# Performance work log

Measured on AMD Instinct MI355X. Metric: run time of the kernel, lower is better.

Reference implementation:

```python
import jax, jax.numpy as jnp
import numpy as np

T = 2.0          # hardcoded in __init__ (self.T = 2)
EPSILON = 0.1    # sinkhorn_loss default
N_ITERS = 10     # sinkhorn_loss default passed to sinkhorn_normalized
COST_CLIP = 10.0
TINY = 1e-8

B, S, V = 16, 512, 4096


def setup_inputs() -> dict:
    key = jax.random.key(0)
    k1, k2 = jax.random.split(key)
    y_s = jax.random.normal(k1, (B, S, V), dtype=jnp.float32)
    y_t = jax.random.normal(k2, (B, S, V), dtype=jnp.float32)
    return {"y_s": y_s, "y_t": y_t}


def _cdist_l1(x, y):
    # x, y: [S, V] -> [S, S]; row-streamed via lax.map to avoid a [S,S,V] intermediate
    return jax.lax.map(lambda xi: jnp.sum(jnp.abs(xi[None, :] - y), axis=-1), x)


def _sinkhorn_loss(x, y):
    # x, y: [S, V] softmax probabilities for one sample
    Wxy = _cdist_l1(x, y)                                  # [S, S]
    K = jnp.exp(-jnp.minimum(Wxy, COST_CLIP) / EPSILON)
    P = jnp.nan_to_num(K, nan=TINY, posinf=1e6, neginf=-1e6) + TINY
    for _ in range(N_ITERS):
        P = P / jnp.maximum(jnp.sum(P, axis=1, keepdims=True), TINY)
        P = jnp.nan_to_num(P, nan=TINY)
        P = P / jnp.maximum(jnp.sum(P, axis=0, keepdims=True), TINY)
        P = jnp.nan_to_num(P, nan=TINY)
    return jnp.sum(P * Wxy)


def reference(y_s, y_t):
    p_s = jax.nn.softmax(y_s / T, axis=-1)
    p_t = jax.nn.softmax(y_t / T, axis=-1)
    p_s = jnp.nan_to_num(p_s, nan=TINY)
    p_t = jnp.nan_to_num(p_t, nan=TINY)
    per_sample = jax.vmap(_sinkhorn_loss)(p_s, p_t)        # [B]
    # forward accumulates 0.001 * loss_i and divides by the number of valid samples
    return jnp.mean(0.001 * per_sample)
```

## Files before the change

kernel.cpp:

```cpp
#include <hip/hip_runtime.h>

#define B_ 16
#define S_ 512
#define V_ 4096

typedef unsigned int uint;
typedef unsigned short ushort;
typedef unsigned char u8;


__device__ __forceinline__ uint sad8(uint a, uint b, uint c) {
#if __has_builtin(__builtin_amdgcn_sad_u8)
    return __builtin_amdgcn_sad_u8(a, b, c);
#else
    uint s = c;
#pragma unroll
    for (int i = 0; i < 4; ++i) {
        uint x = (a >> (8 * i)) & 0xFFu, y = (b >> (8 * i)) & 0xFFu;
        s += x > y ? x - y : y - x;
    }
    return s;
#endif
}

__device__ __forceinline__ float bflo(uint p) { return __uint_as_float(p << 16); }
__device__ __forceinline__ float bfhi(uint p) { return __uint_as_float(p & 0xFFFF0000u); }

__device__ __forceinline__ ushort f2bf(float f) {
    uint u = __float_as_uint(f);
    u = (u + 0x7FFFu + ((u >> 16) & 1u)) >> 16;
    return (ushort)u;
}

__device__ __forceinline__ float waveMax(float v) {
#pragma unroll
    for (int o = 32; o; o >>= 1) v = fmaxf(v, __shfl_xor(v, o, 64));
    return v;
}
__device__ __forceinline__ float waveSum(float v) {
#pragma unroll
    for (int o = 32; o; o >>= 1) v += __shfl_xor(v, o, 64);
    return v;
}

#define GLOAD_LDS16(g, l)                                                      \
    __builtin_amdgcn_global_load_lds(                                          \
        (const __attribute__((address_space(1))) uint*)(g),                    \
        (__attribute__((address_space(3))) uint*)(l), 16, 0, 0)

#define QSCALE 65536.0f
#define QINV   1.52587890625e-5f

__global__ __launch_bounds__(256) void softmax_kernel(
        const float* __restrict__ ys, const float* __restrict__ yt,
        u8* __restrict__ qs, u8* __restrict__ qt) {
    const int row = blockIdx.x;
    const float* in = blockIdx.y ? yt : ys;
    u8* out = blockIdx.y ? qt : qs;
    const float* px = in + (size_t)row * V_;
    u8* po = out + (size_t)row * V_;
    const int tid = threadIdx.x;

    float4 v4[4];
    float m = -3.4e38f;
#pragma unroll
    for (int i = 0; i < 4; ++i) {
        v4[i] = ((const float4*)px)[tid + 256 * i];
        m = fmaxf(m, fmaxf(fmaxf(v4[i].x, v4[i].y), fmaxf(v4[i].z, v4[i].w)));
    }
    __shared__ float redm[4], reds[4];
    float wm = waveMax(m);
    if ((tid & 63) == 0) redm[tid >> 6] = wm;
    __syncthreads();
    const float rm = fmaxf(fmaxf(redm[0], redm[1]), fmaxf(redm[2], redm[3]));

    float e[16];
    float s = 0.f;
#pragma unroll
    for (int i = 0; i < 4; ++i) {
        const float* f = (const float*)&v4[i];
#pragma unroll
        for (int k = 0; k < 4; ++k) {
            float ev = __expf((f[k] - rm) * 0.5f);
            e[i * 4 + k] = ev;
            s += ev;
        }
    }
    float wsm = waveSum(s);
    if ((tid & 63) == 0) reds[tid >> 6] = wsm;
    __syncthreads();
    const float inv = 1.0f / (reds[0] + reds[1] + reds[2] + reds[3]);

#pragma unroll
    for (int i = 0; i < 4; ++i) {
        uint pk = 0;
#pragma unroll
        for (int k = 0; k < 4; ++k) {
            float p = e[i * 4 + k] * inv;
            uint q = (uint)fminf(p * QSCALE + 0.5f, 255.f);
            pk |= q << (8 * k);
        }
        ((uint*)po)[tid + 256 * i] = pk;
    }
}

#define TI 64
#define TJ 64
#define KCB 64

__global__ __launch_bounds__(256) void pairwise_kernel(
        const u8* __restrict__ qs, const u8* __restrict__ qt,
        ushort* __restrict__ Wb, ushort* __restrict__ Kb) {
    const int b = blockIdx.z;
    const int tR = blockIdx.y * TI;
    const int tC = blockIdx.x * TJ;
    const u8* xrow = qs + (size_t)b * S_ * V_ + (size_t)tR * V_;
    const u8* yrow = qt + (size_t)b * S_ * V_ + (size_t)tC * V_;
    const int tid = threadIdx.x;
    const int lane = tid & 63, wv = tid >> 6;
    const int tx = tid & 15, ty = tid >> 4;

    __shared__ u8 xs[2][TI * KCB];
    __shared__ u8 ysm[2][TJ * KCB];

    const int rs = lane >> 2;
    const int coff = (((lane & 3) ^ ((lane >> 3) & 3)) << 4);
    const size_t gsrc = (size_t)(wv * 16 + rs) * V_ + coff;
    const int ldst = wv * 1024;

    uint acc[4][4];
#pragma unroll
    for (int r = 0; r < 4; ++r)
#pragma unroll
        for (int c = 0; c < 4; ++c) acc[r][c] = 0u;

    GLOAD_LDS16(xrow + gsrc, &xs[0][ldst]);
    GLOAD_LDS16(yrow + gsrc, &ysm[0][ldst]);
    __syncthreads();

#pragma unroll 2
    for (int c0 = 0; c0 < V_ / KCB; ++c0) {
        const int cur = c0 & 1;
        if (c0 + 1 < V_ / KCB) {
            const size_t kn = (size_t)(c0 + 1) * KCB;
            GLOAD_LDS16(xrow + kn + gsrc, &xs[cur ^ 1][ldst]);
            GLOAD_LDS16(yrow + kn + gsrc, &ysm[cur ^ 1][ldst]);
        }
#pragma unroll
        for (int kk = 0; kk < 4; ++kk) {
            uint4 Af[4], Bf[4];
#pragma unroll
            for (int r = 0; r < 4; ++r) {
                const int R = ty + 16 * r;
                Af[r] = *(const uint4*)
                    &xs[cur][R * KCB + ((kk ^ ((R >> 1) & 3)) << 4)];
            }
#pragma unroll
            for (int c = 0; c < 4; ++c) {
                const int C = tx + 16 * c;
                Bf[c] = *(const uint4*)
                    &ysm[cur][C * KCB + ((kk ^ ((C >> 1) & 3)) << 4)];
            }
#pragma unroll
            for (int r = 0; r < 4; ++r)
#pragma unroll
                for (int c = 0; c < 4; ++c) {
                    uint t = sad8(Af[r].x, Bf[c].x, acc[r][c]);
                    t = sad8(Af[r].y, Bf[c].y, t);
                    t = sad8(Af[r].z, Bf[c].z, t);
                    acc[r][c] = sad8(Af[r].w, Bf[c].w, t);
                }
        }
        __syncthreads();
    }

#pragma unroll
    for (int r = 0; r < 4; ++r) {
        const int i = tR + ty + 16 * r;
        const size_t base = ((size_t)b * S_ + i) * S_;
#pragma unroll
        for (int c = 0; c < 4; ++c) {
            const int j = tC + tx + 16 * c;
            const float w = fminf((float)acc[r][c] * QINV, 10.f);
            Wb[base + j] = f2bf(w);
            Kb[base + j] = f2bf(__expf(-10.f * w) + 1e-8f);
        }
    }
}

__global__ __launch_bounds__(1024) void sink_block(
        const ushort* __restrict__ Kb, const ushort* __restrict__ Wb,
        float* __restrict__ out) {
    const int b = blockIdx.x;
    const int tid = threadIdx.x, lane = tid & 63, wv = tid >> 6;
    const int ch = lane & 31, rq = lane >> 5;

    __shared__ float vp[S_];
    __shared__ float uls[S_];
    __shared__ float cwp[16][S_];
    __shared__ float redw[16];

    if (tid < S_) { vp[tid] = 1.f; uls[tid] = 1.f; }
    __syncthreads();

    const ushort* Kl = Kb + (size_t)b * S_ * S_;
    const int chB = ch * 16;

    for (int it = 0; it < 10; ++it) {
        const float4 v0 = *(const float4*)&vp[chB];
        const float4 v1 = *(const float4*)&vp[chB + 4];
        const float4 v2 = *(const float4*)&vp[chB + 8];
        const float4 v3 = *(const float4*)&vp[chB + 12];
        float4 c0 = make_float4(0.f, 0.f, 0.f, 0.f);
        float4 c1 = c0, c2 = c0, c3 = c0;

#pragma unroll 2
        for (int g = 0; g < 16; ++g) {
            const int i = wv * 32 + g * 2 + rq;
            const ushort* kp = Kl + (size_t)i * S_ + chB;
            const uint4 ka = *(const uint4*)kp;
            const uint4 kc = *(const uint4*)(kp + 8);
            float d0 = 0.f, d1 = 0.f;
            d0 = fmaf(bflo(ka.x), v0.x, d0); d0 = fmaf(bfhi(ka.x), v0.y, d0);
            d0 = fmaf(bflo(ka.y), v0.z, d0); d0 = fmaf(bfhi(ka.y), v0.w, d0);
            d0 = fmaf(bflo(ka.z), v1.x, d0); d0 = fmaf(bfhi(ka.z), v1.y, d0);
            d0 = fmaf(bflo(ka.w), v1.z, d0); d0 = fmaf(bfhi(ka.w), v1.w, d0);
            d1 = fmaf(bflo(kc.x), v2.x, d1); d1 = fmaf(bfhi(kc.x), v2.y, d1);
            d1 = fmaf(bflo(kc.y), v2.z, d1); d1 = fmaf(bfhi(kc.y), v2.w, d1);
            d1 = fmaf(bflo(kc.z), v3.x, d1); d1 = fmaf(bfhi(kc.z), v3.y, d1);
            d1 = fmaf(bflo(kc.w), v3.z, d1); d1 = fmaf(bfhi(kc.w), v3.w, d1);
            float dot = d0 + d1;
            dot += __shfl_xor(dot, 1, 64);
            dot += __shfl_xor(dot, 2, 64);
            dot += __shfl_xor(dot, 4, 64);
            dot += __shfl_xor(dot, 8, 64);
            dot += __shfl_xor(dot, 16, 64);
            const float up = uls[i];
            const float un = up / fmaxf(up * dot, 1e-8f);
            if (ch == 0) uls[i] = un;
            c0.x = fmaf(un, bflo(ka.x), c0.x); c0.y = fmaf(un, bfhi(ka.x), c0.y);
            c0.z = fmaf(un, bflo(ka.y), c0.z); c0.w = fmaf(un, bfhi(ka.y), c0.w);
            c1.x = fmaf(un, bflo(ka.z), c1.x); c1.y = fmaf(un, bfhi(ka.z), c1.y);
            c1.z = fmaf(un, bflo(ka.w), c1.z); c1.w = fmaf(un, bfhi(ka.w), c1.w);
            c2.x = fmaf(un, bflo(kc.x), c2.x); c2.y = fmaf(un, bfhi(kc.x), c2.y);
            c2.z = fmaf(un, bflo(kc.y), c2.z); c2.w = fmaf(un, bfhi(kc.y), c2.w);
            c3.x = fmaf(un, bflo(kc.z), c3.x); c3.y = fmaf(un, bfhi(kc.z), c3.y);
            c3.z = fmaf(un, bflo(kc.w), c3.z); c3.w = fmaf(un, bfhi(kc.w), c3.w);
        }
        c0.x += __shfl_xor(c0.x, 32, 64); c0.y += __shfl_xor(c0.y, 32, 64);
        c0.z += __shfl_xor(c0.z, 32, 64); c0.w += __shfl_xor(c0.w, 32, 64);
        c1.x += __shfl_xor(c1.x, 32, 64); c1.y += __shfl_xor(c1.y, 32, 64);
        c1.z += __shfl_xor(c1.z, 32, 64); c1.w += __shfl_xor(c1.w, 32, 64);
        c2.x += __shfl_xor(c2.x, 32, 64); c2.y += __shfl_xor(c2.y, 32, 64);
        c2.z += __shfl_xor(c2.z, 32, 64); c2.w += __shfl_xor(c2.w, 32, 64);
        c3.x += __shfl_xor(c3.x, 32, 64); c3.y += __shfl_xor(c3.y, 32, 64);
        c3.z += __shfl_xor(c3.z, 32, 64); c3.w += __shfl_xor(c3.w, 32, 64);
        if (rq == 0) {
            *(float4*)&cwp[wv][chB] = c0;
            *(float4*)&cwp[wv][chB + 4] = c1;
        } else {
            *(float4*)&cwp[wv][chB + 8] = c2;
            *(float4*)&cwp[wv][chB + 12] = c3;
        }
        __syncthreads();
        if (tid < S_) {
            float s = 0.f;
#pragma unroll
            for (int t = 0; t < 16; ++t) s += cwp[t][tid];
            const float vv = vp[tid];
            vp[tid] = vv / fmaxf(vv * s, 1e-8f);
        }
        __syncthreads();
    }

    const float4 v0 = *(const float4*)&vp[chB];
    const float4 v1 = *(const float4*)&vp[chB + 4];
    const float4 v2 = *(const float4*)&vp[chB + 8];
    const float4 v3 = *(const float4*)&vp[chB + 12];
    const ushort* Wl = Wb + (size_t)b * S_ * S_;
    float accl = 0.f;
#pragma unroll 2
    for (int g = 0; g < 16; ++g) {
        const int i = wv * 32 + g * 2 + rq;
        const ushort* kp = Kl + (size_t)i * S_ + chB;
        const ushort* wp = Wl + (size_t)i * S_ + chB;
        const uint4 ka = *(const uint4*)kp;
        const uint4 kc = *(const uint4*)(kp + 8);
        const uint4 wa = *(const uint4*)wp;
        const uint4 wc = *(const uint4*)(wp + 8);
        float r0 = 0.f, r1 = 0.f;
        r0 = fmaf(bflo(ka.x) * v0.x, bflo(wa.x), r0);
        r0 = fmaf(bfhi(ka.x) * v0.y, bfhi(wa.x), r0);
        r0 = fmaf(bflo(ka.y) * v0.z, bflo(wa.y), r0);
        r0 = fmaf(bfhi(ka.y) * v0.w, bfhi(wa.y), r0);
        r0 = fmaf(bflo(ka.z) * v1.x, bflo(wa.z), r0);
        r0 = fmaf(bfhi(ka.z) * v1.y, bfhi(wa.z), r0);
        r0 = fmaf(bflo(ka.w) * v1.z, bflo(wa.w), r0);
        r0 = fmaf(bfhi(ka.w) * v1.w, bfhi(wa.w), r0);
        r1 = fmaf(bflo(kc.x) * v2.x, bflo(wc.x), r1);
        r1 = fmaf(bfhi(kc.x) * v2.y, bfhi(wc.x), r1);
        r1 = fmaf(bflo(kc.y) * v2.z, bflo(wc.y), r1);
        r1 = fmaf(bfhi(kc.y) * v2.w, bfhi(wc.y), r1);
        r1 = fmaf(bflo(kc.z) * v3.x, bflo(wc.z), r1);
        r1 = fmaf(bfhi(kc.z) * v3.y, bfhi(wc.z), r1);
        r1 = fmaf(bflo(kc.w) * v3.z, bflo(wc.w), r1);
        r1 = fmaf(bfhi(kc.w) * v3.w, bfhi(wc.w), r1);
        float rp = r0 + r1;
        rp += __shfl_xor(rp, 1, 64);
        rp += __shfl_xor(rp, 2, 64);
        rp += __shfl_xor(rp, 4, 64);
        rp += __shfl_xor(rp, 8, 64);
        rp += __shfl_xor(rp, 16, 64);
        if (ch == 0) accl = fmaf(uls[i], rp, accl);
    }
    accl += __shfl_xor(accl, 32, 64);
    if (lane == 0) redw[wv] = accl;
    __syncthreads();
    if (tid == 0) {
        float s = 0.f;
#pragma unroll
        for (int t = 0; t < 16; ++t) s += redw[t];
        atomicAdd(out, s * (0.001f / 16.f));
    }
}

extern "C" void kernel_launch(void* const* d_in, const int* in_sizes, int n_in,
                              void* d_out, int out_size, void* d_ws, size_t ws_size,
                              hipStream_t stream) {
    const float* ys = (const float*)d_in[0];
    const float* yt = (const float*)d_in[1];
    float* out = (float*)d_out;

    char* w = (char*)d_ws;
    u8* qs = (u8*)w;
    u8* qt = qs + (size_t)B_ * S_ * V_;
    ushort* Wb = (ushort*)(qt + (size_t)B_ * S_ * V_);
    ushort* Kb = Wb + (size_t)B_ * S_ * S_;

    (void)hipMemsetAsync(out, 0, sizeof(float), stream);

    softmax_kernel<<<dim3(8192, 2), 256, 0, stream>>>(ys, yt, qs, qt);
    pairwise_kernel<<<dim3(8, 8, 16), 256, 0, stream>>>(qs, qt, Wb, Kb);
    sink_block<<<16, 1024, 0, stream>>>(Kb, Wb, out);
}
```

Baseline: 543.6 us.

## Enlarge pairwise L1 tile to 128x128 with 8x8 per-thread register blocking

Doubles the pairwise SAD kernel's output tile and K-chunk to 128, giving each thread an 8x8 accumulator block and rewriting the global-to-LDS staging and XOR swizzle to match. Each loaded byte is now reused across more outputs, which raises arithmetic intensity and cuts LDS and global traffic per SAD. In exchange the grid shrinks to 256 blocks on a GPU with many CUs, per-thread register use grows sharply, and LDS use rises to 64KB per block, so occupancy and latency hiding may suffer.

After: 552.7 us. About the same (+1.7%).

```diff
diff --git a/kernel.cpp b/kernel.cpp
--- a/kernel.cpp
+++ b/kernel.cpp
@@ -104,9 +104,9 @@
     }
 }
 
-#define TI 64
-#define TJ 64
-#define KCB 64
+#define TI 128
+#define TJ 128
+#define KCB 128
 
 __global__ __launch_bounds__(256) void pairwise_kernel(
         const u8* __restrict__ qs, const u8* __restrict__ qt,
@@ -123,48 +123,57 @@
     __shared__ u8 xs[2][TI * KCB];
     __shared__ u8 ysm[2][TJ * KCB];
 
-    const int rs = lane >> 2;
-    const int coff = (((lane & 3) ^ ((lane >> 3) & 3)) << 4);
-    const size_t gsrc = (size_t)(wv * 16 + rs) * V_ + coff;
-    const int ldst = wv * 1024;
-
-    uint acc[4][4];
-#pragma unroll
-    for (int r = 0; r < 4; ++r)
-#pragma unroll
-        for (int c = 0; c < 4; ++c) acc[r][c] = 0u;
-
-    GLOAD_LDS16(xrow + gsrc, &xs[0][ldst]);
-    GLOAD_LDS16(yrow + gsrc, &ysm[0][ldst]);
-    __syncthreads();
-
-#pragma unroll 2
+    const int rs = lane >> 3;
+    const int coff = ((lane & 7) ^ rs) << 4;
+    const int s0 = wv * 4;
+    const size_t g0 = (size_t)((s0 + 0) * 8 + rs) * V_ + coff;
+    const size_t g1 = (size_t)((s0 + 1) * 8 + rs) * V_ + coff;
+    const size_t g2 = (size_t)((s0 + 2) * 8 + rs) * V_ + coff;
+    const size_t g3 = (size_t)((s0 + 3) * 8 + rs) * V_ + coff;
+
+#define STAGE_V6(bufidx, koff)                                                 \
+    {                                                                          \
+        GLOAD_LDS16(xrow + (koff) + g0, &xs[bufidx][(s0 + 0) * 1024]);         \
+        GLOAD_LDS16(xrow + (koff) + g1, &xs[bufidx][(s0 + 1) * 1024]);         \
+        GLOAD_LDS16(xrow + (koff) + g2, &xs[bufidx][(s0 + 2) * 1024]);         \
+        GLOAD_LDS16(xrow + (koff) + g3, &xs[bufidx][(s0 + 3) * 1024]);         \
+        GLOAD_LDS16(yrow + (koff) + g0, &ysm[bufidx][(s0 + 0) * 1024]);        \
+        GLOAD_LDS16(yrow + (koff) + g1, &ysm[bufidx][(s0 + 1) * 1024]);        \
+        GLOAD_LDS16(yrow + (koff) + g2, &ysm[bufidx][(s0 + 2) * 1024]);        \
+        GLOAD_LDS16(yrow + (koff) + g3, &ysm[bufidx][(s0 + 3) * 1024]);        \
+    }
+
+    uint acc[8][8];
+#pragma unroll
+    for (int r = 0; r < 8; ++r)
+#pragma unroll
+        for (int c = 0; c < 8; ++c) acc[r][c] = 0u;
+
+    const int aswz = ty & 7;
+    const int bswz = tx & 7;
+
+    STAGE_V6(0, 0);
+    __syncthreads();
+
     for (int c0 = 0; c0 < V_ / KCB; ++c0) {
         const int cur = c0 & 1;
-        if (c0 + 1 < V_ / KCB) {
-            const size_t kn = (size_t)(c0 + 1) * KCB;
-            GLOAD_LDS16(xrow + kn + gsrc, &xs[cur ^ 1][ldst]);
-            GLOAD_LDS16(yrow + kn + gsrc, &ysm[cur ^ 1][ldst]);
-        }
-#pragma unroll
-        for (int kk = 0; kk < 4; ++kk) {
-            uint4 Af[4], Bf[4];
-#pragma unroll
-            for (int r = 0; r < 4; ++r) {
-                const int R = ty + 16 * r;
-                Af[r] = *(const uint4*)
-                    &xs[cur][R * KCB + ((kk ^ ((R >> 1) & 3)) << 4)];
-            }
-#pragma unroll
-            for (int c = 0; c < 4; ++c) {
-                const int C = tx + 16 * c;
-                Bf[c] = *(const uint4*)
-                    &ysm[cur][C * KCB + ((kk ^ ((C >> 1) & 3)) << 4)];
-            }
-#pragma unroll
-            for (int r = 0; r < 4; ++r)
-#pragma unroll
-                for (int c = 0; c < 4; ++c) {
+        if (c0 + 1 < V_ / KCB)
+            STAGE_V6(cur ^ 1, (size_t)(c0 + 1) * KCB);
+#pragma unroll
+        for (int kk = 0; kk < 8; ++kk) {
+            const int ao = (kk ^ aswz) << 4;
+            const int bo = (kk ^ bswz) << 4;
+            uint4 Af[8], Bf[8];
+#pragma unroll
+            for (int r = 0; r < 8; ++r)
+                Af[r] = *(const uint4*)&xs[cur][(ty + 16 * r) * KCB + ao];
+#pragma unroll
+            for (int c = 0; c < 8; ++c)
+                Bf[c] = *(const uint4*)&ysm[cur][(tx + 16 * c) * KCB + bo];
+#pragma unroll
+            for (int r = 0; r < 8; ++r)
+#pragma unroll
+                for (int c = 0; c < 8; ++c) {
                     uint t = sad8(Af[r].x, Bf[c].x, acc[r][c]);
                     t = sad8(Af[r].y, Bf[c].y, t);
                     t = sad8(Af[r].z, Bf[c].z, t);
@@ -175,17 +184,18 @@
     }
 
 #pragma unroll
-    for (int r = 0; r < 4; ++r) {
+    for (int r = 0; r < 8; ++r) {
         const int i = tR + ty + 16 * r;
         const size_t base = ((size_t)b * S_ + i) * S_;
 #pragma unroll
-        for (int c = 0; c < 4; ++c) {
+        for (int c = 0; c < 8; ++c) {
             const int j = tC + tx + 16 * c;
             const float w = fminf((float)acc[r][c] * QINV, 10.f);
             Wb[base + j] = f2bf(w);
             Kb[base + j] = f2bf(__expf(-10.f * w) + 1e-8f);
         }
     }
+#undef STAGE_V6
 }
 
 __global__ __launch_bounds__(1024) void sink_block(
@@ -340,6 +350,6 @@
     (void)hipMemsetAsync(out, 0, sizeof(float), stream);
 
     softmax_kernel<<<dim3(8192, 2), 256, 0, stream>>>(ys, yt, qs, qt);
-    pairwise_kernel<<<dim3(8, 8, 16), 256, 0, stream>>>(qs, qt, Wb, Kb);
+    pairwise_kernel<<<dim3(4, 4, 16), 256, 0, stream>>>(qs, qt, Wb, Kb);
     sink_block<<<16, 1024, 0, stream>>>(Kb, Wb, out);
 }
```
